# Kernel tuning notes

Measured on AMD Instinct MI355X. Metric: run time of the kernel, lower is better.

Reference implementation:

```python
import jax, jax.numpy as jnp
import numpy as np

N_NODES = 100000


def gcn_conv(x, W, b, src, dst, n):
    # PyG GCNConv: xW, add self-loops, symmetric normalization, scatter-add, +bias
    xw = x @ W                                   # [N, out]
    loop = jnp.arange(n, dtype=src.dtype)
    s = jnp.concatenate([src, loop])             # [E+N]
    d = jnp.concatenate([dst, loop])             # [E+N]
    deg = jax.ops.segment_sum(jnp.ones_like(d, dtype=xw.dtype), d, num_segments=n)
    dis = jnp.where(deg > 0, jax.lax.rsqrt(jnp.maximum(deg, 1e-12)), 0.0)
    norm = dis[s] * dis[d]                       # [E+N]
    msg = xw[s] * norm[:, None]                  # [E+N, out]  (gather + scale)
    out = jax.ops.segment_sum(msg, d, num_segments=n)  # scatter-add
    return out + b


def setup_inputs() -> dict:
    key = jax.random.key(0)
    k1, k2, k3, k4 = jax.random.split(key, 4)
    x = jax.random.normal(k1, (N_NODES, 128), dtype=jnp.float32)
    edge_index = jax.random.randint(k2, (2, 1600000), 0, N_NODES, dtype=jnp.int64)
    W1 = jax.random.normal(k3, (128, 64), dtype=jnp.float32) * (1.0 / np.sqrt(128))
    b1 = jnp.zeros((64,), dtype=jnp.float32)
    W2 = jax.random.normal(k4, (64, 40), dtype=jnp.float32) * (1.0 / np.sqrt(64))
    b2 = jnp.zeros((40,), dtype=jnp.float32)
    return {"x": x, "edge_index": edge_index, "W1": W1, "b1": b1, "W2": W2, "b2": b2}


def reference(x, edge_index, W1, b1, W2, b2):
    src, dst = edge_index[0], edge_index[1]
    n = x.shape[0]
    h = gcn_conv(x, W1, b1, src, dst, n)
    h = jax.nn.relu(h)
    # dropout p=0.6 is identity in eval mode (training=False)
    h = gcn_conv(h, W2, b2, src, dst, n)
    return jax.nn.log_softmax(h, axis=1)
```

## Files before the change

kernel.cpp:

```cpp
#include <hip/hip_runtime.h>
#include <math.h>

typedef unsigned short u16;
typedef unsigned int u32;
typedef __attribute__((ext_vector_type(2))) float f32x2;

#define CAP 64
#define BSHIFT 9
#define BCAP 9600

__device__ inline float bf2f(u16 u) {
    union { u32 i; float f; } c; c.i = ((u32)u) << 16; return c.f;
}
__device__ inline u32 cvtpk(float lo, float hi) {
    u32 r;
    asm("v_cvt_pk_bf16_f32 %0, %1, %2" : "=v"(r) : "v"(lo), "v"(hi));
    return r;
}
__device__ inline f32x2 unp(u32 d) {
    union { u32 u; float f; } lo, hi;
    lo.u = d << 16;
    hi.u = d & 0xFFFF0000u;
    f32x2 r; r.x = lo.f; r.y = hi.f;
    return r;
}
__device__ inline f32x2 shflx2(f32x2 val, int m) {
    union { f32x2 v; int u[2]; } a; a.v = val;
    a.u[0] = __shfl_xor(a.u[0], m);
    a.u[1] = __shfl_xor(a.u[1], m);
    return a.v;
}


__global__ void zero_gcount_kernel(int* __restrict__ gcount) {
    gcount[threadIdx.x] = 0;
}

__global__ __launch_bounds__(256) void bucket_kernel(const int* __restrict__ src,
                                                     const int* __restrict__ dst,
                                                     int* __restrict__ gcount,
                                                     int2* __restrict__ bucketbuf,
                                                     int e, int nb) {
    __shared__ int lh[256];
    int tid = threadIdx.x;
    if (tid < nb) lh[tid] = 0;
    __syncthreads();
    int per = (e + gridDim.x - 1) / gridDim.x;
    int i0 = blockIdx.x * per;
    int i1 = i0 + per; if (i1 > e) i1 = e;
    for (int i = i0 + tid; i < i1; i += 256)
        atomicAdd(&lh[dst[i] >> BSHIFT], 1);
    __syncthreads();
    if (tid < nb) {
        int c = lh[tid];
        lh[tid] = (c > 0) ? atomicAdd(&gcount[tid], c) : 0;
    }
    __syncthreads();
    for (int i = i0 + tid; i < i1; i += 256) {
        int d = dst[i], s = src[i];
        int b = d >> BSHIFT;
        int pos = atomicAdd(&lh[b], 1);
        if (pos < BCAP) bucketbuf[(size_t)b * BCAP + pos] = make_int2(d, s);
    }
}

__global__ __launch_bounds__(256) void csrify_kernel(const int2* __restrict__ bucketbuf,
                                                     const int* __restrict__ gcount,
                                                     int* __restrict__ cnt,
                                                     float* __restrict__ dis,
                                                     int* __restrict__ srcs2d, int n) {
    __shared__ int lc[512];
    int b = blockIdx.x;
    int tid = threadIdx.x;
    int node_lo = b << BSHIFT;
    #pragma unroll
    for (int q = tid; q < 512; q += 256) lc[q] = 0;
    __syncthreads();
    int m = gcount[b]; if (m > BCAP) m = BCAP;
    const int2* bp = bucketbuf + (size_t)b * BCAP;
    for (int i = tid; i < m; i += 256) {
        int2 r = bp[i];
        int k = atomicAdd(&lc[r.x - node_lo], 1);
        if (k < CAP - 1) srcs2d[((size_t)r.x << 6) + k + 1] = r.y;
    }
    __syncthreads();
    for (int q = tid; q < 512; q += 256) {
        int node = node_lo + q;
        if (node < n) {
            int c = lc[q];
            int nr = (c < CAP - 1 ? c : CAP - 1) + 1;
            cnt[node] = nr;
            dis[node] = rsqrtf((float)c + 1.0f);
            int* row = srcs2d + ((size_t)node << 6);
            row[0] = node;
            int pr = (nr + 7) & ~7;
            for (int t = nr; t < pr; ++t) row[t] = n;
        }
    }
}


__device__ inline float4 load4(const float* p) { return *(const float4*)p; }
__device__ inline float4 load4(const u16* p) {
    ushort4 u = *(const ushort4*)p;
    return make_float4(bf2f(u.x), bf2f(u.y), bf2f(u.z), bf2f(u.w));
}

template<typename XT, int IN_F, int OUT_F, int OSTR>
__global__ __launch_bounds__(256) void gemm_scale_kernel(const XT* __restrict__ X,
                                                         const float* __restrict__ W,
                                                         const float* __restrict__ dis,
                                                         u16* __restrict__ Y, int n) {
    constexpr int PC = 64;
    __shared__ float Wl[IN_F * PC];
    int tid = threadIdx.x;
    for (int idx = tid; idx < IN_F * PC; idx += 256) {
        int k = idx / PC, c = idx % PC;
        Wl[idx] = (c < OUT_F) ? W[k * OUT_F + c] : 0.f;
    }
    __syncthreads();
    int tx = tid & 15;
    int ty = tid >> 4;
    int r0 = blockIdx.x * 64 + ty * 4;
    int c0 = tx * 4;
    const XT* xr[4];
    #pragma unroll
    for (int i = 0; i < 4; ++i) {
        int r = r0 + i;
        if (r >= n) r = n - 1;
        xr[i] = X + (size_t)r * IN_F;
    }
    float acc[4][4] = {};
    const float4* Wv = (const float4*)Wl;
    #pragma unroll 1
    for (int k = 0; k < IN_F; k += 4) {
        float4 xv[4];
        #pragma unroll
        for (int i = 0; i < 4; ++i) xv[i] = load4(xr[i] + k);
        #pragma unroll
        for (int j = 0; j < 4; ++j) {
            float4 wv = Wv[(k + j) * 16 + tx];
            #pragma unroll
            for (int i = 0; i < 4; ++i) {
                float xs = (j == 0) ? xv[i].x : (j == 1) ? xv[i].y : (j == 2) ? xv[i].z : xv[i].w;
                acc[i][0] = fmaf(xs, wv.x, acc[i][0]);
                acc[i][1] = fmaf(xs, wv.y, acc[i][1]);
                acc[i][2] = fmaf(xs, wv.z, acc[i][2]);
                acc[i][3] = fmaf(xs, wv.w, acc[i][3]);
            }
        }
    }
    #pragma unroll
    for (int i = 0; i < 4; ++i) {
        int r = r0 + i;
        if (r < n) {
            float sc = dis[r];
            u32 p0 = cvtpk(acc[i][0] * sc, acc[i][1] * sc);
            u32 p1 = cvtpk(acc[i][2] * sc, acc[i][3] * sc);
            *(uint2*)(Y + (size_t)r * OSTR + c0) = make_uint2(p0, p1);
        } else if (r == n) {
            *(uint2*)(Y + (size_t)r * OSTR + c0) = make_uint2(0u, 0u);
        }
    }
}


template<int FINAL>
__global__ __launch_bounds__(256) void gatherw_kernel(const u16* __restrict__ v,
                                                      const int* __restrict__ cnt,
                                                      const int* __restrict__ srcs2d,
                                                      const float* __restrict__ dis,
                                                      const float* __restrict__ bias,
                                                      u16* __restrict__ outb,
                                                      float* __restrict__ outf, int n) {
    int wid = __builtin_amdgcn_readfirstlane((blockIdx.x * blockDim.x + threadIdx.x) >> 6);
    int lane = threadIdx.x & 63;
    if (wid >= n) return;
    int nrows = __builtin_amdgcn_readfirstlane(cnt[wid]);
    int padded = (nrows + 7) & ~7;
    int j = lane >> 3;
    int c = lane & 7;
    int idx_all = srcs2d[((size_t)wid << 6) + lane];
    f32x2 acc[4];
    #pragma unroll
    for (int i = 0; i < 4; ++i) { acc[i].x = 0.f; acc[i].y = 0.f; }
    int baddr = j << 2;
    u32 coff = (u32)(c << 3);
    for (int k = 0; k < padded; k += 8) {
        int sj = __builtin_amdgcn_ds_bpermute(baddr, idx_all);
        baddr += 32;
        const uint4* rp = (const uint4*)(v + (((u32)sj << 6) + coff));
        uint4 a = *rp;
        acc[0] += unp(a.x);
        acc[1] += unp(a.y);
        acc[2] += unp(a.z);
        acc[3] += unp(a.w);
    }
    #pragma unroll
    for (int i = 0; i < 4; ++i) {
        acc[i] += shflx2(acc[i], 8);
        acc[i] += shflx2(acc[i], 16);
        acc[i] += shflx2(acc[i], 32);
    }
    float di = dis[wid];
    if (FINAL == 0) {
        const f32x2* bp2 = (const f32x2*)(bias + (c << 3));
        f32x2 o[4];
        #pragma unroll
        for (int i = 0; i < 4; ++i) {
            f32x2 b = bp2[i];
            o[i].x = fmaxf(fmaf(di, acc[i].x, b.x), 0.f);
            o[i].y = fmaxf(fmaf(di, acc[i].y, b.y), 0.f);
        }
        if (j == 0) {
            uint4 p = make_uint4(cvtpk(o[0].x, o[0].y), cvtpk(o[1].x, o[1].y),
                                 cvtpk(o[2].x, o[2].y), cvtpk(o[3].x, o[3].y));
            *(uint4*)(outb + (((size_t)wid) << 6) + (c << 3)) = p;
        }
    } else {
        bool act = c < 5;
        int cb = act ? c : 0;
        const f32x2* bp2 = (const f32x2*)(bias + (cb << 3));
        float zz[8];
        #pragma unroll
        for (int i = 0; i < 4; ++i) {
            f32x2 b = bp2[i];
            zz[2 * i]     = act ? fmaf(di, acc[i].x, b.x) : -INFINITY;
            zz[2 * i + 1] = act ? fmaf(di, acc[i].y, b.y) : -INFINITY;
        }
        float mx = zz[0];
        #pragma unroll
        for (int i = 1; i < 8; ++i) mx = fmaxf(mx, zz[i]);
        mx = fmaxf(mx, __shfl_xor(mx, 1));
        mx = fmaxf(mx, __shfl_xor(mx, 2));
        mx = fmaxf(mx, __shfl_xor(mx, 4));
        float ssum = 0.f;
        if (act) {
            #pragma unroll
            for (int i = 0; i < 8; ++i) ssum += __expf(zz[i] - mx);
        }
        ssum += __shfl_xor(ssum, 1);
        ssum += __shfl_xor(ssum, 2);
        ssum += __shfl_xor(ssum, 4);
        float ls = __logf(ssum) + mx;
        if (j == 0 && act) {
            float* op = outf + (size_t)wid * 40 + (c << 3);
            *(float4*)op = make_float4(zz[0] - ls, zz[1] - ls, zz[2] - ls, zz[3] - ls);
            *(float4*)(op + 4) = make_float4(zz[4] - ls, zz[5] - ls, zz[6] - ls, zz[7] - ls);
        }
    }
}


extern "C" void kernel_launch(void* const* d_in, const int* in_sizes, int n_in,
                              void* d_out, int out_size, void* d_ws, size_t ws_size,
                              hipStream_t stream) {
    const float* x  = (const float*)d_in[0];
    const int*   ei = (const int*)d_in[1];
    const float* W1 = (const float*)d_in[2];
    const float* b1 = (const float*)d_in[3];
    const float* W2 = (const float*)d_in[4];
    const float* b2 = (const float*)d_in[5];
    float* out = (float*)d_out;

    const int n = in_sizes[0] / 128;
    const int e = in_sizes[1] / 2;
    const int* src = ei;
    const int* dst = ei + e;
    const int nb = (n + 511) >> BSHIFT;

    int* gcount = (int*)d_ws;
    int* cnt    = gcount + 256;
    float* dis  = (float*)(cnt + n);
    int2* bucketbuf = (int2*)(dis + n);
    u16* A      = (u16*)bucketbuf;
    int* srcs2d = (int*)(bucketbuf + (size_t)nb * BCAP);
    u16* B      = (u16*)(srcs2d + ((size_t)n << 6));

    const int T = 256;
    const int gblocks = (n * 64 + T - 1) / T;
    const int mblocks = (n >> 6) + 1;

    zero_gcount_kernel<<<1, 256, 0, stream>>>(gcount);
    bucket_kernel<<<448, 256, 0, stream>>>(src, dst, gcount, bucketbuf, e, nb);
    csrify_kernel<<<nb, 256, 0, stream>>>(bucketbuf, gcount, cnt, dis, srcs2d, n);

    gemm_scale_kernel<float, 128, 64, 64>
        <<<mblocks, 256, 0, stream>>>(x, W1, dis, A, n);
    gatherw_kernel<0><<<gblocks, T, 0, stream>>>(A, cnt, srcs2d, dis, b1, B, nullptr, n);

    gemm_scale_kernel<u16, 64, 40, 64>
        <<<mblocks, 256, 0, stream>>>(B, W2, dis, A, n);
    gatherw_kernel<1><<<gblocks, T, 0, stream>>>(A, cnt, srcs2d, dis, b2, nullptr, out, n);
}
```

Baseline: 290.4 us.

## Replace scalar FMA dense transforms with bf16 MFMA matrix-core kernel

Rewrites both dense feature-transform GEMMs to use 16x16x32 bf16 MFMA instructions. Weights are transposed into bf16 in shared memory and held as register fragments, while fp32 inputs are packed to bf16 on load. Each block now covers 128 rows instead of 64. This lowers the compute cost of the GEMMs, but the first layer's input is now rounded to bf16 before the multiply, and outputs are written as scattered 16-bit stores rather than vector stores.

Result: faster. 271.1 us (-6.6%).

```diff
diff --git a/kernel.cpp b/kernel.cpp
--- a/kernel.cpp
+++ b/kernel.cpp
@@ -4,6 +4,8 @@
 typedef unsigned short u16;
 typedef unsigned int u32;
 typedef __attribute__((ext_vector_type(2))) float f32x2;
+typedef __attribute__((ext_vector_type(4))) float f32x4;
+typedef __attribute__((ext_vector_type(8))) short short8;
 
 #define CAP 64
 #define BSHIFT 9
@@ -11,6 +13,11 @@
 
 __device__ inline float bf2f(u16 u) {
     union { u32 i; float f; } c; c.i = ((u32)u) << 16; return c.f;
+}
+__device__ inline u16 f2bf(float f) {
+    union { float f; u32 i; } c; c.f = f;
+    u32 r = c.i + 0x7FFFu + ((c.i >> 16) & 1u);
+    return (u16)(r >> 16);
 }
 __device__ inline u32 cvtpk(float lo, float hi) {
     u32 r;
@@ -100,66 +107,87 @@
 }
 
 
-__device__ inline float4 load4(const float* p) { return *(const float4*)p; }
-__device__ inline float4 load4(const u16* p) {
-    ushort4 u = *(const ushort4*)p;
-    return make_float4(bf2f(u.x), bf2f(u.y), bf2f(u.z), bf2f(u.w));
-}
-
-template<typename XT, int IN_F, int OUT_F, int OSTR>
-__global__ __launch_bounds__(256) void gemm_scale_kernel(const XT* __restrict__ X,
-                                                         const float* __restrict__ W,
-                                                         const float* __restrict__ dis,
-                                                         u16* __restrict__ Y, int n) {
-    constexpr int PC = 64;
-    __shared__ float Wl[IN_F * PC];
+template<typename XT, int IN_F, int OUT_F>
+__global__ __launch_bounds__(256) void gemm_mfma_kernel(const XT* __restrict__ X,
+                                                        const float* __restrict__ W,
+                                                        const float* __restrict__ dis,
+                                                        u16* __restrict__ Y, int n) {
+    constexpr int KP = IN_F + 8;
+    constexpr int NKS = IN_F / 32;
+    __shared__ u16 Wt[64 * KP];
     int tid = threadIdx.x;
-    for (int idx = tid; idx < IN_F * PC; idx += 256) {
-        int k = idx / PC, c = idx % PC;
-        Wl[idx] = (c < OUT_F) ? W[k * OUT_F + c] : 0.f;
-    }
-    __syncthreads();
-    int tx = tid & 15;
-    int ty = tid >> 4;
-    int r0 = blockIdx.x * 64 + ty * 4;
-    int c0 = tx * 4;
-    const XT* xr[4];
-    #pragma unroll
-    for (int i = 0; i < 4; ++i) {
-        int r = r0 + i;
-        if (r >= n) r = n - 1;
-        xr[i] = X + (size_t)r * IN_F;
-    }
-    float acc[4][4] = {};
-    const float4* Wv = (const float4*)Wl;
-    #pragma unroll 1
-    for (int k = 0; k < IN_F; k += 4) {
-        float4 xv[4];
-        #pragma unroll
-        for (int i = 0; i < 4; ++i) xv[i] = load4(xr[i] + k);
+    for (int idx = tid; idx < 64 * IN_F; idx += 256) {
+        int c = idx / IN_F, k = idx % IN_F;
+        float v = (c < OUT_F) ? W[k * OUT_F + c] : 0.f;
+        Wt[c * KP + k] = f2bf(v);
+    }
+    __syncthreads();
+    int l = tid & 63;
+    int w = tid >> 6;
+    int lm = l & 15;
+    int g4 = (l >> 4) << 2;
+
+    short8 Bf[4][NKS];
+    #pragma unroll
+    for (int ct = 0; ct < 4; ++ct) {
+        const u16* wp = &Wt[(ct * 16 + lm) * KP + g4];
+        #pragma unroll
+        for (int ks = 0; ks < NKS; ++ks) {
+            union { short8 s; uint2 u[2]; } b;
+            b.u[0] = *(const uint2*)(wp + ks * 32);
+            b.u[1] = *(const uint2*)(wp + ks * 32 + 16);
+            Bf[ct][ks] = b.s;
+        }
+    }
+
+    #pragma unroll
+    for (int rt = 0; rt < 2; ++rt) {
+        int rw = blockIdx.x * 128 + rt * 64 + w * 16;
+        int ra = rw + lm;
+        if (ra >= n) ra = n - 1;
+        short8 Af[NKS];
+        if (sizeof(XT) == 4) {
+            const float* xp = (const float*)X + (size_t)ra * IN_F + g4;
+            #pragma unroll
+            for (int ks = 0; ks < NKS; ++ks) {
+                float4 f1 = *(const float4*)(xp + ks * 32);
+                float4 f2 = *(const float4*)(xp + ks * 32 + 16);
+                union { short8 s; u32 d[4]; } a;
+                a.d[0] = cvtpk(f1.x, f1.y);
+                a.d[1] = cvtpk(f1.z, f1.w);
+                a.d[2] = cvtpk(f2.x, f2.y);
+                a.d[3] = cvtpk(f2.z, f2.w);
+                Af[ks] = a.s;
+            }
+        } else {
+            const u16* xp = (const u16*)X + (size_t)ra * IN_F + g4;
+            #pragma unroll
+            for (int ks = 0; ks < NKS; ++ks) {
+                union { short8 s; uint2 u[2]; } a;
+                a.u[0] = *(const uint2*)(xp + ks * 32);
+                a.u[1] = *(const uint2*)(xp + ks * 32 + 16);
+                Af[ks] = a.s;
+            }
+        }
+        f32x4 acc[4] = {};
+        #pragma unroll
+        for (int ks = 0; ks < NKS; ++ks)
+            #pragma unroll
+            for (int ct = 0; ct < 4; ++ct)
+                acc[ct] = __builtin_amdgcn_mfma_f32_16x16x32_bf16(Af[ks], Bf[ct][ks], acc[ct], 0, 0, 0);
         #pragma unroll
         for (int j = 0; j < 4; ++j) {
-            float4 wv = Wv[(k + j) * 16 + tx];
-            #pragma unroll
-            for (int i = 0; i < 4; ++i) {
-                float xs = (j == 0) ? xv[i].x : (j == 1) ? xv[i].y : (j == 2) ? xv[i].z : xv[i].w;
-                acc[i][0] = fmaf(xs, wv.x, acc[i][0]);
-                acc[i][1] = fmaf(xs, wv.y, acc[i][1]);
-                acc[i][2] = fmaf(xs, wv.z, acc[i][2]);
-                acc[i][3] = fmaf(xs, wv.w, acc[i][3]);
+            int r = rw + ((l >> 4) << 2) + j;
+            if (r < n) {
+                float sc = dis[r];
+                #pragma unroll
+                for (int ct = 0; ct < 4; ++ct)
+                    Y[(size_t)r * 64 + ct * 16 + lm] = f2bf(acc[ct][j] * sc);
+            } else if (r == n) {
+                #pragma unroll
+                for (int ct = 0; ct < 4; ++ct)
+                    Y[(size_t)r * 64 + ct * 16 + lm] = 0;
             }
-        }
-    }
-    #pragma unroll
-    for (int i = 0; i < 4; ++i) {
-        int r = r0 + i;
-        if (r < n) {
-            float sc = dis[r];
-            u32 p0 = cvtpk(acc[i][0] * sc, acc[i][1] * sc);
-            u32 p1 = cvtpk(acc[i][2] * sc, acc[i][3] * sc);
-            *(uint2*)(Y + (size_t)r * OSTR + c0) = make_uint2(p0, p1);
-        } else if (r == n) {
-            *(uint2*)(Y + (size_t)r * OSTR + c0) = make_uint2(0u, 0u);
         }
     }
 }
@@ -279,17 +307,17 @@
 
     const int T = 256;
     const int gblocks = (n * 64 + T - 1) / T;
-    const int mblocks = (n >> 6) + 1;
+    const int mblocks = (n + 128) / 128;
 
     zero_gcount_kernel<<<1, 256, 0, stream>>>(gcount);
     bucket_kernel<<<448, 256, 0, stream>>>(src, dst, gcount, bucketbuf, e, nb);
     csrify_kernel<<<nb, 256, 0, stream>>>(bucketbuf, gcount, cnt, dis, srcs2d, n);
 
-    gemm_scale_kernel<float, 128, 64, 64>
+    gemm_mfma_kernel<float, 128, 64>
         <<<mblocks, 256, 0, stream>>>(x, W1, dis, A, n);
     gatherw_kernel<0><<<gblocks, T, 0, stream>>>(A, cnt, srcs2d, dis, b1, B, nullptr, n);
 
-    gemm_scale_kernel<u16, 64, 40, 64>
+    gemm_mfma_kernel<u16, 64, 40>
         <<<mblocks, 256, 0, stream>>>(B, W2, dis, A, n);
     gatherw_kernel<1><<<gblocks, T, 0, stream>>>(A, cnt, srcs2d, dis, b2, nullptr, out, n);
 }
```
